# Kernel optimization log

Measured on AMD Instinct MI355X. Metric: run time of the kernel, lower is better.

Reference implementation:

```python
import jax, jax.numpy as jnp
import numpy as np

NUM_MODELS = 64
OUT_F = 256
IN_F = 256
B = 32768
F0 = 2
F1 = 2


def setup_inputs() -> dict:
    key = jax.random.key(0)
    k1, k2, k3, k4 = jax.random.split(key, 4)
    sqrt_k = float(np.sqrt(1.0 / NUM_MODELS))
    weights = 2 * sqrt_k * jax.random.uniform(k1, (NUM_MODELS, OUT_F, IN_F), dtype=jnp.float32) - sqrt_k
    biases = 2 * sqrt_k * jax.random.uniform(k2, (NUM_MODELS, OUT_F), dtype=jnp.float32) - sqrt_k
    inputs = jax.random.normal(k3, (B, IN_F // F1), dtype=jnp.float32)
    indices = jax.random.randint(k4, (B,), 0, NUM_MODELS, dtype=jnp.int64)
    return {"inputs": inputs, "weights": weights, "biases": biases,
            "indices": indices, "factor0": F0, "factor1": F1}


def reference(inputs, weights, biases, indices, factor0, factor1):
    out_sub = weights.shape[1] // factor0
    in_sub = weights.shape[2] // factor1
    # Gather per-sample weight slices: (B, out_sub, in_sub)
    subweight = weights[indices, :out_sub, :in_sub]
    subbias = biases[indices, :out_sub]  # (B, out_sub)
    # Batched matvec + bias
    return jnp.einsum('boi,bi->bo', subweight, inputs) + subbias
```

## Files before the change

### kernel.cpp

```cpp
#include <hip/hip_runtime.h>
#include <hip/hip_bf16.h>

#define NMODELS 64
#define NB      32768
#define INF     256
#define OUTF    256
#define INS     128
#define OUTS    128
#define TILE_M  64
#define NT      8
#define NSB     128
#define WCONV_BLOCKS 512
#define POISON  0xAAAAAAAAu

typedef unsigned int u32;
typedef unsigned short u16;
using bf16x8  = __attribute__((ext_vector_type(8))) short;
using f32x4   = __attribute__((ext_vector_type(4))) float;
using float4v = __attribute__((ext_vector_type(4))) float;
using short8v = __attribute__((ext_vector_type(8))) short;

__device__ __forceinline__ u16 f2bf(float f) {
    union { float fv; u32 u; } v; v.fv = f;
    u32 u = v.u;
    u += 0x7fffu + ((u >> 16) & 1u);
    return (u16)(u >> 16);
}

__device__ __forceinline__ void async_copy16(const void* g, void* l) {
    __builtin_amdgcn_global_load_lds((const __attribute__((address_space(1))) u32*)g,
                                     (__attribute__((address_space(3))) u32*)l,
                                     16, 0, 0);
}

__global__ __launch_bounds__(256) void k_scatconv(const int* __restrict__ idx,
                                                  const float* __restrict__ w,
                                                  u32* __restrict__ cursors,
                                                  int* __restrict__ perm,
                                                  u16* __restrict__ wb) {
    const int t = threadIdx.x;
    const int b = blockIdx.x;
    if (b < NSB) {
        __shared__ int h[NMODELS];
        __shared__ int base[NMODELS];
        const int i = b * 256 + t;
        const int m = idx[i];
        if (t < NMODELS) h[t] = 0;
        __syncthreads();
        const int r = atomicAdd(&h[m], 1);
        __syncthreads();
        if (t < NMODELS && h[t] != 0)
            base[t] = (int)(atomicAdd(&cursors[t], (u32)h[t]) - POISON);
        __syncthreads();
        perm[(m << 10) + base[m] + r] = i;
    } else {
        const int cid = (b - NSB) * 256 + t;
        const int m   = cid >> 11;
        const int rem = cid & 2047;
        const int row = rem >> 4;
        const int c   = rem & 15;
        const float* src = w + ((size_t)m * OUTF + row) * INF + c * 8;
        float4v v0 = *(const float4v*)(src);
        float4v v1 = *(const float4v*)(src + 4);
        short8v s;
        s[0]=(short)f2bf(v0.x); s[1]=(short)f2bf(v0.y); s[2]=(short)f2bf(v0.z); s[3]=(short)f2bf(v0.w);
        s[4]=(short)f2bf(v1.x); s[5]=(short)f2bf(v1.y); s[6]=(short)f2bf(v1.z); s[7]=(short)f2bf(v1.w);
        *(short8v*)(wb + ((size_t)(m * 128 + row) * 128) + ((c ^ (row & 15)) * 8)) = s;
    }
}

__global__ __launch_bounds__(256) void k_gemm(const float* __restrict__ x,
                                              const u16* __restrict__ wb,
                                              const float* __restrict__ bias,
                                              const u32* __restrict__ cursors,
                                              const int* __restrict__ perm,
                                              float* __restrict__ out) {
    __shared__ __align__(16) u16 Ws[OUTS * 128];
    const int m    = blockIdx.x;
    const int t    = threadIdx.x;
    const int wave = t >> 6;
    const int lane = t & 63;
    const int quad = lane >> 4;
    const int lr   = lane & 15;

    {
        const char* g = (const char*)(wb + (size_t)m * (OUTS * 128));
        char* l = (char*)Ws;
        #pragma unroll
        for (int itc = 0; itc < 8; ++itc) {
            const int off = itc * 4096 + wave * 1024;
            async_copy16(g + off + lane * 16, l + off);
        }
    }

    const int pbase = m << 10;
    int tile = blockIdx.y;
    int row  = tile * TILE_M + wave * 16 + lr;
    int p    = perm[pbase + row];
    const int cnt = (int)(cursors[m] - POISON);
    int  pidx = p & (NB - 1);
    bool v    = row < cnt;

    const float* xr = x + (size_t)pidx * INS + quad * 8;
    float4v xa[8];
    #pragma unroll
    for (int k0 = 0; k0 < 4; ++k0) {
        xa[2 * k0]     = *(const float4v*)(xr + k0 * 32);
        xa[2 * k0 + 1] = *(const float4v*)(xr + k0 * 32 + 4);
    }

    float4v bv4[8];
    #pragma unroll
    for (int nt = 0; nt < 8; ++nt)
        bv4[nt] = *(const float4v*)(bias + m * OUTF + nt * 16 + quad * 4);

    int xoff[4];
    #pragma unroll
    for (int k0 = 0; k0 < 4; ++k0) xoff[k0] = ((k0 * 4 + quad) ^ lr) * 8;
    const int rowbase = lr * 128;

    __syncthreads();

    for (;;) {
        bf16x8 xb[4];
        #pragma unroll
        for (int k0 = 0; k0 < 4; ++k0) {
            bf16x8 a;
            a[0] = (short)f2bf(xa[2*k0].x);   a[1] = (short)f2bf(xa[2*k0].y);
            a[2] = (short)f2bf(xa[2*k0].z);   a[3] = (short)f2bf(xa[2*k0].w);
            a[4] = (short)f2bf(xa[2*k0+1].x); a[5] = (short)f2bf(xa[2*k0+1].y);
            a[6] = (short)f2bf(xa[2*k0+1].z); a[7] = (short)f2bf(xa[2*k0+1].w);
            xb[k0] = a;
        }
        f32x4 acc[8];
        #pragma unroll
        for (int nt = 0; nt < 8; ++nt) acc[nt] = (f32x4){0.f, 0.f, 0.f, 0.f};
        #pragma unroll
        for (int k0 = 0; k0 < 4; ++k0) {
            #pragma unroll
            for (int nt = 0; nt < 8; ++nt) {
                bf16x8 wfr = *(const bf16x8*)&Ws[nt * 2048 + rowbase + xoff[k0]];
                acc[nt] = __builtin_amdgcn_mfma_f32_16x16x32_bf16(wfr, xb[k0], acc[nt], 0, 0, 0);
            }
        }
        const int  curpi = pidx;
        const bool curv  = v;
        const int  ntile = tile + NT;
        const bool more  = (ntile * TILE_M < cnt);
        if (more) {
            row  = ntile * TILE_M + wave * 16 + lr;
            p    = perm[pbase + row];
            pidx = p & (NB - 1);
            v    = row < cnt;
            const float* xr2 = x + (size_t)pidx * INS + quad * 8;
            #pragma unroll
            for (int k0 = 0; k0 < 4; ++k0) {
                xa[2 * k0]     = *(const float4v*)(xr2 + k0 * 32);
                xa[2 * k0 + 1] = *(const float4v*)(xr2 + k0 * 32 + 4);
            }
        }
        if (curv) {
            float* orow = out + (size_t)curpi * OUTS + quad * 4;
            #pragma unroll
            for (int nt = 0; nt < 8; ++nt)
                *(float4v*)(orow + nt * 16) = acc[nt] + bv4[nt];
        }
        if (!more) break;
        tile = ntile;
    }
}

extern "C" void kernel_launch(void* const* d_in, const int* in_sizes, int n_in,
                              void* d_out, int out_size, void* d_ws, size_t ws_size,
                              hipStream_t stream) {
    const float* x    = (const float*)d_in[0];
    const float* w    = (const float*)d_in[1];
    const float* bias = (const float*)d_in[2];
    const int*   idx  = (const int*)d_in[3];
    float* out = (float*)d_out;

    int* ws      = (int*)d_ws;
    u32* cursors = (u32*)ws;
    int* perm    = ws + 64;
    u16* wb      = (u16*)(ws + 64 + 65536);

    k_scatconv<<<dim3(NSB + WCONV_BLOCKS), dim3(256), 0, stream>>>(idx, w, cursors, perm, wb);
    k_gemm    <<<dim3(NMODELS, NT),        dim3(256), 0, stream>>>(x, wb, bias, cursors, perm, out);
}
```

Before: 94.15 us.

## Fuse weight fp32-to-bf16 conversion into GEMM kernel, drop staging buffer

Moves the fp32-to-bf16 weight conversion out of the scatter kernel and into the GEMM kernel. Each GEMM block now loads its model's 128x128 fp32 weight slice, converts it in registers and writes it swizzled into LDS. This removes the bf16 weight round trip through global memory and the larger first kernel. In exchange, each of the 8 blocks per model repeats the conversion, loads 2x more bytes per block, and gives up the async global-to-LDS copy. It also adds a 2-blocks-per-CU launch bound.

```diff
diff --git a/kernel.cpp b/kernel.cpp
--- a/kernel.cpp
+++ b/kernel.cpp
@@ -10,7 +10,6 @@
 #define TILE_M  64
 #define NT      8
 #define NSB     128
-#define WCONV_BLOCKS 512
 #define POISON  0xAAAAAAAAu
 
 typedef unsigned int u32;
@@ -27,54 +26,30 @@
     return (u16)(u >> 16);
 }
 
-__device__ __forceinline__ void async_copy16(const void* g, void* l) {
-    __builtin_amdgcn_global_load_lds((const __attribute__((address_space(1))) u32*)g,
-                                     (__attribute__((address_space(3))) u32*)l,
-                                     16, 0, 0);
+__global__ __launch_bounds__(256) void k_scat(const int* __restrict__ idx,
+                                              u32* __restrict__ cursors,
+                                              int* __restrict__ perm) {
+    __shared__ int h[NMODELS];
+    __shared__ int base[NMODELS];
+    const int t = threadIdx.x;
+    const int i = blockIdx.x * 256 + t;
+    const int m = idx[i];
+    if (t < NMODELS) h[t] = 0;
+    __syncthreads();
+    const int r = atomicAdd(&h[m], 1);
+    __syncthreads();
+    if (t < NMODELS && h[t] != 0)
+        base[t] = (int)(atomicAdd(&cursors[t], (u32)h[t]) - POISON);
+    __syncthreads();
+    perm[(m << 10) + base[m] + r] = i;
 }
 
-__global__ __launch_bounds__(256) void k_scatconv(const int* __restrict__ idx,
-                                                  const float* __restrict__ w,
-                                                  u32* __restrict__ cursors,
-                                                  int* __restrict__ perm,
-                                                  u16* __restrict__ wb) {
-    const int t = threadIdx.x;
-    const int b = blockIdx.x;
-    if (b < NSB) {
-        __shared__ int h[NMODELS];
-        __shared__ int base[NMODELS];
-        const int i = b * 256 + t;
-        const int m = idx[i];
-        if (t < NMODELS) h[t] = 0;
-        __syncthreads();
-        const int r = atomicAdd(&h[m], 1);
-        __syncthreads();
-        if (t < NMODELS && h[t] != 0)
-            base[t] = (int)(atomicAdd(&cursors[t], (u32)h[t]) - POISON);
-        __syncthreads();
-        perm[(m << 10) + base[m] + r] = i;
-    } else {
-        const int cid = (b - NSB) * 256 + t;
-        const int m   = cid >> 11;
-        const int rem = cid & 2047;
-        const int row = rem >> 4;
-        const int c   = rem & 15;
-        const float* src = w + ((size_t)m * OUTF + row) * INF + c * 8;
-        float4v v0 = *(const float4v*)(src);
-        float4v v1 = *(const float4v*)(src + 4);
-        short8v s;
-        s[0]=(short)f2bf(v0.x); s[1]=(short)f2bf(v0.y); s[2]=(short)f2bf(v0.z); s[3]=(short)f2bf(v0.w);
-        s[4]=(short)f2bf(v1.x); s[5]=(short)f2bf(v1.y); s[6]=(short)f2bf(v1.z); s[7]=(short)f2bf(v1.w);
-        *(short8v*)(wb + ((size_t)(m * 128 + row) * 128) + ((c ^ (row & 15)) * 8)) = s;
-    }
-}
-
-__global__ __launch_bounds__(256) void k_gemm(const float* __restrict__ x,
-                                              const u16* __restrict__ wb,
-                                              const float* __restrict__ bias,
-                                              const u32* __restrict__ cursors,
-                                              const int* __restrict__ perm,
-                                              float* __restrict__ out) {
+__global__ __launch_bounds__(256, 2) void k_gemm(const float* __restrict__ x,
+                                                 const float* __restrict__ w,
+                                                 const float* __restrict__ bias,
+                                                 const u32* __restrict__ cursors,
+                                                 const int* __restrict__ perm,
+                                                 float* __restrict__ out) {
     __shared__ __align__(16) u16 Ws[OUTS * 128];
     const int m    = blockIdx.x;
     const int t    = threadIdx.x;
@@ -83,14 +58,16 @@
     const int quad = lane >> 4;
     const int lr   = lane & 15;
 
-    {
-        const char* g = (const char*)(wb + (size_t)m * (OUTS * 128));
-        char* l = (char*)Ws;
-        #pragma unroll
-        for (int itc = 0; itc < 8; ++itc) {
-            const int off = itc * 4096 + wave * 1024;
-            async_copy16(g + off + lane * 16, l + off);
-        }
+    const float* wsrc = w + (size_t)m * (OUTF * INF);
+    float4v wv[16];
+    #pragma unroll
+    for (int it = 0; it < 8; ++it) {
+        const int cid = (it << 8) + t;
+        const int row = cid >> 4;
+        const int c   = cid & 15;
+        const float* src = wsrc + row * INF + (c << 3);
+        wv[2 * it]     = *(const float4v*)(src);
+        wv[2 * it + 1] = *(const float4v*)(src + 4);
     }
 
     const int pbase = m << 10;
@@ -98,9 +75,22 @@
     int row  = tile * TILE_M + wave * 16 + lr;
     int p    = perm[pbase + row];
     const int cnt = (int)(cursors[m] - POISON);
+
+    #pragma unroll
+    for (int it = 0; it < 8; ++it) {
+        const int cid = (it << 8) + t;
+        const int row2 = cid >> 4;
+        const int c    = cid & 15;
+        short8v s;
+        s[0]=(short)f2bf(wv[2*it].x);   s[1]=(short)f2bf(wv[2*it].y);
+        s[2]=(short)f2bf(wv[2*it].z);   s[3]=(short)f2bf(wv[2*it].w);
+        s[4]=(short)f2bf(wv[2*it+1].x); s[5]=(short)f2bf(wv[2*it+1].y);
+        s[6]=(short)f2bf(wv[2*it+1].z); s[7]=(short)f2bf(wv[2*it+1].w);
+        *(short8v*)&Ws[(row2 << 7) + ((c ^ (row2 & 15)) << 3)] = s;
+    }
+
     int  pidx = p & (NB - 1);
     bool v    = row < cnt;
-
     const float* xr = x + (size_t)pidx * INS + quad * 8;
     float4v xa[8];
     #pragma unroll
@@ -108,7 +98,6 @@
         xa[2 * k0]     = *(const float4v*)(xr + k0 * 32);
         xa[2 * k0 + 1] = *(const float4v*)(xr + k0 * 32 + 4);
     }
-
     float4v bv4[8];
     #pragma unroll
     for (int nt = 0; nt < 8; ++nt)
@@ -182,8 +171,7 @@
     int* ws      = (int*)d_ws;
     u32* cursors = (u32*)ws;
     int* perm    = ws + 64;
-    u16* wb      = (u16*)(ws + 64 + 65536);
 
-    k_scatconv<<<dim3(NSB + WCONV_BLOCKS), dim3(256), 0, stream>>>(idx, w, cursors, perm, wb);
-    k_gemm    <<<dim3(NMODELS, NT),        dim3(256), 0, stream>>>(x, wb, bias, cursors, perm, out);
+    k_scat<<<dim3(NSB),        dim3(256), 0, stream>>>(idx, cursors, perm);
+    k_gemm<<<dim3(NMODELS, NT), dim3(256), 0, stream>>>(x, w, bias, cursors, perm, out);
 }
```

Result: faster. 91.90 us (-2.4%).
